# Kernel optimization log

Hardware: AMD Instinct MI355X
Metric: run time of the kernel (lower is better)

## Reference

```python
import jax, jax.numpy as jnp
import numpy as np

NUM_GROUPS = 8
NUM_HEADS = 4
EPS = 1e-5


def group_norm(x, w, b):
    # x: [B, C, H, W]; normalize over (C/G, H, W) within each of G groups
    B, C, H, W = x.shape
    xg = x.reshape(B, NUM_GROUPS, C // NUM_GROUPS, H, W)
    mean = xg.mean(axis=(2, 3, 4), keepdims=True)
    var = xg.var(axis=(2, 3, 4), keepdims=True)
    xn = ((xg - mean) * jax.lax.rsqrt(var + EPS)).reshape(B, C, H, W)
    return xn * w[None, :, None, None] + b[None, :, None, None]


def setup_inputs() -> dict:
    key = jax.random.key(0)
    ks = jax.random.split(key, 7)
    B, C, H, W = 4, 256, 64, 64
    x = jax.random.normal(ks[0], (B, C, H, W), dtype=jnp.float32)
    gn_w = jax.random.normal(ks[1], (C,), dtype=jnp.float32) * 0.1 + 1.0
    gn_b = jax.random.normal(ks[2], (C,), dtype=jnp.float32) * 0.1
    qkv_w = jax.random.normal(ks[3], (3 * C, C), dtype=jnp.float32) / np.sqrt(C)
    qkv_b = jax.random.normal(ks[4], (3 * C,), dtype=jnp.float32) * 0.02
    proj_w = jax.random.normal(ks[5], (C, C), dtype=jnp.float32) / np.sqrt(C)
    proj_b = jax.random.normal(ks[6], (C,), dtype=jnp.float32) * 0.02
    return {"x": x, "gn_w": gn_w, "gn_b": gn_b, "qkv_w": qkv_w,
            "qkv_b": qkv_b, "proj_w": proj_w, "proj_b": proj_b}


def reference(x, gn_w, gn_b, qkv_w, qkv_b, proj_w, proj_b):
    B, C, H, W = x.shape
    nh = NUM_HEADS
    hd = C // nh
    scale = hd ** -0.5
    N = H * W

    h = group_norm(x, gn_w, gn_b)
    # 1x1 conv == channel matmul: [B, 3C, H, W]
    qkv = jnp.einsum('oc,bchw->bohw', qkv_w, h) + qkv_b[None, :, None, None]
    qkv = qkv.reshape(B, 3, nh, hd, N)  # matches torch .view(B,3,nh,hd,HW)
    q, k, v = qkv[:, 0], qkv[:, 1], qkv[:, 2]  # each [B, nh, hd, N]

    attn = jnp.einsum('bhdn,bhdm->bhnm', q, k) * scale  # [B, nh, N, N]
    attn = jax.nn.softmax(attn, axis=-1)
    out = jnp.einsum('bhnm,bhdm->bhdn', attn, v)  # [B, nh, hd, N]
    out = out.reshape(B, C, H, W)

    proj = jnp.einsum('oc,bchw->bohw', proj_w, out) + proj_b[None, :, None, None]
    return x + proj
```

## Files before the change

kernel.cpp:

```cpp
#include <hip/hip_runtime.h>
#include <hip/hip_bf16.h>

#define BB   4
#define CC   256
#define NN   4096
#define NH   4
#define HD   64
#define NG   8
#define GSZ  32
#define EPSV 1e-5f
#define SCALE_L2E 0.18033688f

typedef __bf16 bf16x8 __attribute__((ext_vector_type(8)));
typedef float  f32x4  __attribute__((ext_vector_type(4)));

#define MFMA16(a, b, c)  __builtin_amdgcn_mfma_f32_16x16x32_bf16((a), (b), (c), 0, 0, 0)

#if __has_builtin(__builtin_amdgcn_exp2f)
#define EXP2F __builtin_amdgcn_exp2f
#else
#define EXP2F exp2f
#endif

#define WAITV(n)  asm volatile("s_waitcnt vmcnt(" #n ")" ::: "memory")
#define WAITL0    asm volatile("s_waitcnt lgkmcnt(0)" ::: "memory")
#define SBAR      __builtin_amdgcn_s_barrier()
#define SCHED0    __builtin_amdgcn_sched_barrier(0)

__device__ inline unsigned short f2bf(float f) {
    unsigned int u = __float_as_uint(f);
    u += 0x7fffu + ((u >> 16) & 1u);
    return (unsigned short)(u >> 16);
}

__device__ __forceinline__ bf16x8 pk8(const f32x4& p0, const f32x4& p1) {
    alignas(16) unsigned int u[4];
    u[0] = __builtin_amdgcn_perm(__float_as_uint(p0[1]), __float_as_uint(p0[0]), 0x07060302u);
    u[1] = __builtin_amdgcn_perm(__float_as_uint(p0[3]), __float_as_uint(p0[2]), 0x07060302u);
    u[2] = __builtin_amdgcn_perm(__float_as_uint(p1[1]), __float_as_uint(p1[0]), 0x07060302u);
    u[3] = __builtin_amdgcn_perm(__float_as_uint(p1[3]), __float_as_uint(p1[2]), 0x07060302u);
    return *reinterpret_cast<bf16x8*>(u);
}

__device__ __forceinline__ void async_ld16(void* lds, const void* g) {
    __builtin_amdgcn_global_load_lds(
        (const __attribute__((address_space(1))) unsigned int*)g,
        (__attribute__((address_space(3))) unsigned int*)lds, 16, 0, 0);
}

__global__ void k_prep(const float* __restrict__ x, float* __restrict__ stats,
                       const float* __restrict__ wp, unsigned short* __restrict__ op) {
    int blk = blockIdx.x;
    int t = threadIdx.x;
    if (blk >= 256) {
        int i = (blk - 256) * 256 + t;
        if (i < CC * CC) op[i] = f2bf(wp[i]);
        return;
    }
    int b = blk >> 6, g = (blk >> 3) & 7, s = blk & 7;
    const float* p = x + ((size_t)(b * CC + g * GSZ)) * NN + s * 16384;
    float s0 = 0.f, s1 = 0.f;
    #pragma unroll
    for (int i = 0; i < 64; ++i) { float v = p[i * 256 + t]; s0 += v; s1 += v * v; }
    #pragma unroll
    for (int m = 1; m <= 32; m <<= 1) { s0 += __shfl_xor(s0, m); s1 += __shfl_xor(s1, m); }
    __shared__ float ls[8];
    int w = t >> 6;
    if ((t & 63) == 0) { ls[w * 2] = s0; ls[w * 2 + 1] = s1; }
    __syncthreads();
    if (t == 0) {
        float a0 = ls[0] + ls[2] + ls[4] + ls[6];
        float a1 = ls[1] + ls[3] + ls[5] + ls[7];
        stats[((b * NG + g) * 8 + s) * 2 + 0] = a0;
        stats[((b * NG + g) * 8 + s) * 2 + 1] = a1;
    }
}

__global__ void __launch_bounds__(256)
k_tab(const float* __restrict__ wq, const float* __restrict__ gw, const float* __restrict__ gb,
      const float* __restrict__ qb, const float* __restrict__ stats,
      unsigned short* __restrict__ wqp, float* __restrict__ biasq) {
    int o = blockIdx.x, b = blockIdx.y, c = threadIdx.x;
    int g = c >> 5;
    float s0 = 0.f, s1 = 0.f;
    #pragma unroll
    for (int s = 0; s < 8; ++s) {
        s0 += stats[((b * NG + g) * 8 + s) * 2 + 0];
        s1 += stats[((b * NG + g) * 8 + s) * 2 + 1];
    }
    float mean = s0 * (1.0f / 131072.0f);
    float var  = s1 * (1.0f / 131072.0f) - mean * mean;
    float inv  = rsqrtf(var + EPSV);
    float Ac = gw[c] * inv;
    float Bc = gb[c] - mean * Ac;
    float w = wq[o * CC + c];
    wqp[((size_t)b * 768 + o) * CC + c] = f2bf(w * Ac);
    float p = w * Bc;
    #pragma unroll
    for (int m = 1; m <= 32; m <<= 1) p += __shfl_xor(p, m);
    __shared__ float ls[4];
    if ((c & 63) == 0) ls[c >> 6] = p;
    __syncthreads();
    if (c == 0) biasq[b * 768 + o] = qb[o] + ls[0] + ls[1] + ls[2] + ls[3];
}

__global__ void __launch_bounds__(256)
k_qkv(const float* __restrict__ x, const unsigned short* __restrict__ wqp,
      const float* __restrict__ biasq,
      unsigned short* __restrict__ qt, unsigned short* __restrict__ kt,
      unsigned short* __restrict__ vt) {
    int bx = blockIdx.x, by = blockIdx.y;
    int t = threadIdx.x, wave = t >> 6, lane = t & 63;
    int l15 = lane & 15, quad = lane >> 4;
    int wm = wave >> 1, wn = wave & 1;

    __shared__ alignas(16) unsigned char smem[49152];

    int nn0 = bx * 128;
    int b = nn0 >> 12, nbase = nn0 & 4095;

    const char* Ag = (const char*)wqp + (size_t)b * 393216 + (size_t)by * 65536;
    int row0 = t >> 2, slot = t & 3;
    size_t a0 = (size_t)row0 * 512 + slot * 16;
    size_t a1 = a0 + 64 * 512;
    unsigned int dstA = wave * 1024;

    int colsrc = (((lane & 31) * 16) - 32 * wave) & 511;
    const char* xrow = (const char*)x +
        (((size_t)(b * CC) + (wave * 8 + (lane >> 5))) * NN + nbase) * 4 + colsrc;

    auto stage = [&](int buf, int kk) {
        async_ld16(smem + buf * 8192 + dstA,        Ag + a0 + (size_t)kk * 64);
        async_ld16(smem + buf * 8192 + 4096 + dstA, Ag + a1 + (size_t)kk * 64);
        const char* bs = xrow + (size_t)kk * 32 * NN * 4;
        unsigned char* bd = smem + 16384 + buf * 16384 + wave * 4096;
        async_ld16(bd,        bs);
        async_ld16(bd + 1024, bs + (size_t)2 * NN * 4);
        async_ld16(bd + 2048, bs + (size_t)4 * NN * 4);
        async_ld16(bd + 3072, bs + (size_t)6 * NN * 4);
    };

    int colr[4];
    #pragma unroll
    for (int f = 0; f < 4; ++f)
        colr[f] = (((wn * 64 + f * 16 + l15) * 4) + quad * 32) & 511;

    f32x4 acc[4][4];
    #pragma unroll
    for (int i = 0; i < 4; ++i)
        #pragma unroll
        for (int j = 0; j < 4; ++j) acc[i][j] = (f32x4){0.f, 0.f, 0.f, 0.f};

    stage(0, 0);
    stage(1, 1);

    for (int kk = 0; kk < 8; ++kk) {
        if (kk < 7) { WAITV(6); } else { WAITV(0); }
        SCHED0;
        SBAR;
        SCHED0;
        int cur = kk & 1;
        bf16x8 af[4], bf[4];
        #pragma unroll
        for (int f = 0; f < 4; ++f)
            af[f] = *reinterpret_cast<const bf16x8*>(smem + cur * 8192 + (wm * 64 + f * 16 + l15) * 64 + quad * 16);
        #pragma unroll
        for (int f = 0; f < 4; ++f) {
            const unsigned char* fb = smem + 16384 + cur * 16384 + quad * 4096 + colr[f];
            alignas(16) unsigned int u[4];
            #pragma unroll
            for (int jj = 0; jj < 4; ++jj) {
                float xl = *reinterpret_cast<const float*>(fb + (2 * jj) * 512);
                float xh = *reinterpret_cast<const float*>(fb + (2 * jj + 1) * 512);
                asm("v_cvt_pk_bf16_f32 %0, %1, %2" : "=v"(u[jj]) : "v"(xl), "v"(xh));
            }
            bf[f] = *reinterpret_cast<const bf16x8*>(u);
        }
        #pragma unroll
        for (int fm = 0; fm < 4; ++fm)
            #pragma unroll
            for (int fn = 0; fn < 4; ++fn)
                acc[fm][fn] = MFMA16(af[fm], bf[fn], acc[fm][fn]);
        WAITL0;
        SCHED0;
        SBAR;
        SCHED0;
        if (kk < 6) stage(cur, kk + 2);
    }

    int s = by >> 1;
    if (s < 2) {
        #pragma unroll
        for (int fm = 0; fm < 4; ++fm) {
            int o = by * 128 + wm * 64 + fm * 16 + quad * 4;
            int h = (o >> 6) & 3, d0 = o & 63;
            float bias[4];
            #pragma unroll
            for (int r = 0; r < 4; ++r) bias[r] = biasq[b * 768 + o + r];
            #pragma unroll
            for (int fn = 0; fn < 4; ++fn) {
                int n = nbase + wn * 64 + fn * 16 + l15;
                alignas(8) unsigned short o4[4];
                if (s == 0) {
                    #pragma unroll
                    for (int r = 0; r < 4; ++r) o4[r] = f2bf((acc[fm][fn][r] + bias[r]) * SCALE_L2E);
                    *reinterpret_cast<uint2*>(qt + (((size_t)(b * NH + h) * NN) + n) * HD + d0) =
                        *reinterpret_cast<const uint2*>(o4);
                } else {
                    #pragma unroll
                    for (int r = 0; r < 4; ++r) o4[r] = f2bf(acc[fm][fn][r] + bias[r]);
                    *reinterpret_cast<uint2*>(kt + (((size_t)(b * NH + h) * NN) + n) * HD + d0) =
                        *reinterpret_cast<const uint2*>(o4);
                }
            }
        }
    } else {
        unsigned short* vtile = (unsigned short*)smem;
        #pragma unroll
        for (int fm = 0; fm < 4; ++fm) {
            int o  = by * 128 + wm * 64 + fm * 16 + quad * 4;
            int ol = wm * 64 + fm * 16 + quad * 4;
            float bias[4];
            #pragma unroll
            for (int r = 0; r < 4; ++r) bias[r] = biasq[b * 768 + o + r];
            #pragma unroll
            for (int fn = 0; fn < 4; ++fn) {
                int nl = wn * 64 + fn * 16 + l15;
                #pragma unroll
                for (int r = 0; r < 4; ++r)
                    vtile[(ol + r) * 132 + nl] = f2bf(acc[fm][fn][r] + bias[r]);
            }
        }
        __syncthreads();
        int hbase = (by - 4) * 2;
        #pragma unroll
        for (int pass = 0; pass < 8; ++pass) {
            int row  = pass * 16 + (t >> 4);
            int col0 = (t & 15) * 8;
            int nb = (col0 & ~31) | ((col0 & 16) >> 1) | ((col0 & 8) >> 1);
            const unsigned short* src = vtile + row * 132 + nb;
            uint2 lo = *reinterpret_cast<const uint2*>(src);
            uint2 hi = *reinterpret_cast<const uint2*>(src + 16);
            uint4 o4 = make_uint4(lo.x, lo.y, hi.x, hi.y);
            int h = hbase + (row >> 6), d = row & 63;
            *reinterpret_cast<uint4*>(vt + ((size_t)(b * NH + h) * HD + d) * NN + nbase + col0) = o4;
        }
    }
}

__global__ void __launch_bounds__(256, 4)
k_attn(const unsigned short* __restrict__ qt, const unsigned short* __restrict__ kt,
       const unsigned short* __restrict__ vt,
       unsigned short* __restrict__ op0, unsigned short* __restrict__ op1,
       float* __restrict__ lip) {
    int bh = blockIdx.y;
    int split = blockIdx.z;
    int t = threadIdx.x, wave = t >> 6, lane = t & 63;
    int l15 = lane & 15, quad = lane >> 4;
    int qbase = blockIdx.x * 128 + wave * 32;
    int kbase = split * 2048;
    const unsigned short* qp = qt + (size_t)bh * NN * HD;
    const unsigned short* kp = kt + (size_t)bh * NN * HD;
    const unsigned short* vp = vt + (size_t)bh * HD * NN;

    __shared__ alignas(16) unsigned char kbuf[2][8192];
    __shared__ alignas(16) unsigned char vbuf[2][8192];

    int lr8 = lane >> 3, lc8 = lane & 7;
    int swz = lc8 ^ lr8;
    const char* ksrc = (const char*)kp + (size_t)(kbase + wave * 16 + lr8) * 128 + swz * 16;
    const char* vsrc = (const char*)vp + (size_t)(wave * 16 + lr8) * 8192 + (size_t)kbase * 2 + swz * 16;
    unsigned int dstw = wave * 2048;

    auto stage = [&](int buf) {
        async_ld16(kbuf[buf] + dstw,        ksrc);
        async_ld16(kbuf[buf] + dstw + 1024, ksrc + 1024);
        ksrc += 8192;
        async_ld16(vbuf[buf] + dstw,        vsrc);
        async_ld16(vbuf[buf] + dstw + 1024, vsrc + 8 * 8192);
        vsrc += 128;
    };

    bf16x8 qaA0 = *reinterpret_cast<const bf16x8*>(qp + (size_t)(qbase + l15) * HD + quad * 8);
    bf16x8 qaA1 = *reinterpret_cast<const bf16x8*>(qp + (size_t)(qbase + l15) * HD + 32 + quad * 8);
    bf16x8 qaB0 = *reinterpret_cast<const bf16x8*>(qp + (size_t)(qbase + 16 + l15) * HD + quad * 8);
    bf16x8 qaB1 = *reinterpret_cast<const bf16x8*>(qp + (size_t)(qbase + 16 + l15) * HD + 32 + quad * 8);

    const f32x4 Z4 = (f32x4){0.f, 0.f, 0.f, 0.f};
    bf16x8 vone;
    #pragma unroll
    for (int i = 0; i < 8; ++i) vone[i] = (__bf16)1.0f;

    f32x4 OA[4], OB[4];
    #pragma unroll
    for (int i = 0; i < 4; ++i) { OA[i] = Z4; OB[i] = Z4; }
    f32x4 liAA = Z4, liBB = Z4;

    int sx = l15 & 7;

    auto compute = [&](const unsigned char* kb, const unsigned char* vbb) {
        f32x4 sA0[2], sA1[2], sB0[2], sB1[2];
        __builtin_amdgcn_s_setprio(1);
        #pragma unroll
        for (int s = 0; s < 2; ++s) {
            int r0 = (s * 32 + l15) * 128;
            bf16x8 k00 = *reinterpret_cast<const bf16x8*>(kb + r0 + ((quad ^ sx) * 16));
            bf16x8 k01 = *reinterpret_cast<const bf16x8*>(kb + r0 + (((quad + 4) ^ sx) * 16));
            bf16x8 k10 = *reinterpret_cast<const bf16x8*>(kb + r0 + 2048 + ((quad ^ sx) * 16));
            bf16x8 k11 = *reinterpret_cast<const bf16x8*>(kb + r0 + 2048 + (((quad + 4) ^ sx) * 16));
            sA0[s] = MFMA16(k00, qaA0, Z4);  sA0[s] = MFMA16(k01, qaA1, sA0[s]);
            sA1[s] = MFMA16(k10, qaA0, Z4);  sA1[s] = MFMA16(k11, qaA1, sA1[s]);
            sB0[s] = MFMA16(k00, qaB0, Z4);  sB0[s] = MFMA16(k01, qaB1, sB0[s]);
            sB1[s] = MFMA16(k10, qaB0, Z4);  sB1[s] = MFMA16(k11, qaB1, sB1[s]);
        }
        __builtin_amdgcn_s_setprio(0);
        #pragma unroll
        for (int s = 0; s < 2; ++s) {
            f32x4 pA0, pA1, pB0, pB1;
            #pragma unroll
            for (int r = 0; r < 4; ++r) {
                pA0[r] = EXP2F(sA0[s][r]);  pA1[r] = EXP2F(sA1[s][r]);
                pB0[r] = EXP2F(sB0[s][r]);  pB1[r] = EXP2F(sB1[s][r]);
            }
            bf16x8 fA = pk8(pA0, pA1);
            bf16x8 fB = pk8(pB0, pB1);

            __builtin_amdgcn_s_setprio(1);
            liAA = MFMA16(fA, vone, liAA);
            liBB = MFMA16(fB, vone, liBB);

            #pragma unroll
            for (int dc = 0; dc < 4; ++dc) {
                const unsigned char* vrow = vbb + (dc * 16 + l15) * 128;
                bf16x8 vv = *reinterpret_cast<const bf16x8*>(vrow + (((s * 4 + quad) ^ sx) * 16));
                OA[dc] = MFMA16(fA, vv, OA[dc]);
                OB[dc] = MFMA16(fB, vv, OB[dc]);
            }
            __builtin_amdgcn_s_setprio(0);
        }
    };

    stage(0);
    __syncthreads();

    for (int p = 0; p < 16; ++p) {
        stage(1);
        compute(kbuf[0], vbuf[0]);
        __syncthreads();
        if (p < 15) stage(0);
        compute(kbuf[1], vbuf[1]);
        __syncthreads();
    }

    unsigned short* op = split ? op1 : op0;
    int b = bh >> 2, h = bh & 3;
    #pragma unroll
    for (int dc = 0; dc < 4; ++dc) {
        #pragma unroll
        for (int r = 0; r < 4; ++r) {
            int qA = qbase + quad * 4 + r;
            op[((size_t)(b * NN) + qA) * CC + h * HD + dc * 16 + l15]      = f2bf(OA[dc][r]);
            op[((size_t)(b * NN) + qA + 16) * CC + h * HD + dc * 16 + l15] = f2bf(OB[dc][r]);
        }
    }
    float* lp = lip + (size_t)split * (16 * NN) + (size_t)bh * NN + qbase;
    if (l15 == 0) {
        #pragma unroll
        for (int r = 0; r < 4; ++r) {
            lp[quad * 4 + r]      = liAA[r];
            lp[16 + quad * 4 + r] = liBB[r];
        }
    }
}

__global__ void __launch_bounds__(256)
k_proj(const unsigned short* __restrict__ ao, const unsigned short* __restrict__ p1,
       const float* __restrict__ lip,
       const unsigned short* __restrict__ wp, const float* __restrict__ pb,
       const float* __restrict__ x, float* __restrict__ out) {
    int bx = blockIdx.x, by = blockIdx.y;
    int t = threadIdx.x, wave = t >> 6, lane = t & 63;
    int l15 = lane & 15, quad = lane >> 4;
    int wm = wave >> 1, wn = wave & 1;

    __shared__ alignas(16) unsigned char At[2][4096];
    __shared__ alignas(16) unsigned char Bt[2][4096];

    const char* Ag = (const char*)wp + (size_t)by * 32768;
    int row0 = t >> 2, slot = t & 3;
    size_t a0 = (size_t)row0 * 512 + slot * 16;
    unsigned int dst0 = wave * 1024;

    int gtok = bx * 64 + row0;
    int b = gtok >> 12, n = gtok & 4095;
    size_t obase = ((size_t)(b * NN) + n) * CC + slot * 8;
    float inv[4];
    #pragma unroll
    for (int h = 0; h < 4; ++h) {
        size_t lb = (size_t)(b * 4 + h) * NN + n;
        inv[h] = 1.0f / (lip[lb] + lip[lb + (size_t)16 * NN]);
    }

    auto stageA = [&](int buf, int kk) {
        async_ld16(At[buf] + dst0, Ag + a0 + (size_t)kk * 64);
    };
    uint4 eu0, eu1, ou0, ou1;
    auto loadB = [&](uint4& r0, uint4& r1, int kk) {
        r0 = *reinterpret_cast<const uint4*>(ao + obase + kk * 32);
        r1 = *reinterpret_cast<const uint4*>(p1 + obase + kk * 32);
    };
    auto writeB = [&](int buf, const uint4& r0, const uint4& r1, float iv) {
        const unsigned short* q0 = reinterpret_cast<const unsigned short*>(&r0);
        const unsigned short* q1 = reinterpret_cast<const unsigned short*>(&r1);
        alignas(16) unsigned short o8[8];
        #pragma unroll
        for (int i = 0; i < 8; ++i) {
            float f0 = __uint_as_float((unsigned)q0[i] << 16);
            float f1 = __uint_as_float((unsigned)q1[i] << 16);
            o8[i] = f2bf((f0 + f1) * iv);
        }
        *reinterpret_cast<uint4*>(Bt[buf] + row0 * 64 + slot * 16) =
            *reinterpret_cast<const uint4*>(o8);
    };

    f32x4 acc[2][2];
    #pragma unroll
    for (int i = 0; i < 2; ++i)
        #pragma unroll
        for (int j = 0; j < 2; ++j) acc[i][j] = (f32x4){0.f, 0.f, 0.f, 0.f};

    loadB(eu0, eu1, 0);
    stageA(0, 0);
    loadB(ou0, ou1, 1);

    #pragma unroll
    for (int k2 = 0; k2 < 4; ++k2) {
        {
            const int kk = 2 * k2;
            WAITV(2);
            SCHED0;
            writeB(0, eu0, eu1, inv[kk >> 1]);
            WAITL0;
            SCHED0;
            SBAR;
            SCHED0;
            if (kk < 7) stageA(1, kk + 1);
            if (kk < 6) loadB(eu0, eu1, kk + 2);
            bf16x8 af[2], bf[2];
            #pragma unroll
            for (int f = 0; f < 2; ++f) {
                af[f] = *reinterpret_cast<const bf16x8*>(At[0] + (wm * 32 + f * 16 + l15) * 64 + quad * 16);
                bf[f] = *reinterpret_cast<const bf16x8*>(Bt[0] + (wn * 32 + f * 16 + l15) * 64 + quad * 16);
            }
            #pragma unroll
            for (int fm = 0; fm < 2; ++fm)
                #pragma unroll
                for (int fn = 0; fn < 2; ++fn)
                    acc[fm][fn] = MFMA16(af[fm], bf[fn], acc[fm][fn]);
        }
        {
            const int kk = 2 * k2 + 1;
            if (kk < 7) { WAITV(2); } else { WAITV(0); }
            SCHED0;
            writeB(1, ou0, ou1, inv[kk >> 1]);
            WAITL0;
            SCHED0;
            SBAR;
            SCHED0;
            if (kk < 7) stageA(0, kk + 1);
            if (kk < 6) loadB(ou0, ou1, kk + 2);
            bf16x8 af[2], bf[2];
            #pragma unroll
            for (int f = 0; f < 2; ++f) {
                af[f] = *reinterpret_cast<const bf16x8*>(At[1] + (wm * 32 + f * 16 + l15) * 64 + quad * 16);
                bf[f] = *reinterpret_cast<const bf16x8*>(Bt[1] + (wn * 32 + f * 16 + l15) * 64 + quad * 16);
            }
            #pragma unroll
            for (int fm = 0; fm < 2; ++fm)
                #pragma unroll
                for (int fn = 0; fn < 2; ++fn)
                    acc[fm][fn] = MFMA16(af[fm], bf[fn], acc[fm][fn]);
        }
    }

    int nn0 = bx * 64;
    int bb = nn0 >> 12, nbase = nn0 & 4095;
    #pragma unroll
    for (int fm = 0; fm < 2; ++fm) {
        int o = by * 64 + wm * 32 + fm * 16 + quad * 4;
        float bias[4];
        #pragma unroll
        for (int r = 0; r < 4; ++r) bias[r] = pb[o + r];
        #pragma unroll
        for (int fn = 0; fn < 2; ++fn) {
            int nc = nbase + wn * 32 + fn * 16 + l15;
            #pragma unroll
            for (int r = 0; r < 4; ++r) {
                size_t idx = ((size_t)(bb * CC + o + r)) * NN + nc;
                out[idx] = acc[fm][fn][r] + bias[r] + x[idx];
            }
        }
    }
}

extern "C" void kernel_launch(void* const* d_in, const int* in_sizes, int n_in,
                              void* d_out, int out_size, void* d_ws, size_t ws_size,
                              hipStream_t stream) {
    const float* x     = (const float*)d_in[0];
    const float* gw    = (const float*)d_in[1];
    const float* gb    = (const float*)d_in[2];
    const float* qkvw  = (const float*)d_in[3];
    const float* qkvb  = (const float*)d_in[4];
    const float* projw = (const float*)d_in[5];
    const float* projb = (const float*)d_in[6];
    float* out = (float*)d_out;

    char* w = (char*)d_ws;
    size_t off = 0;
    unsigned short* qt = (unsigned short*)(w + off); off += (size_t)BB * NH * NN * HD * 2;
    unsigned short* kt = (unsigned short*)(w + off); off += (size_t)BB * NH * NN * HD * 2;
    unsigned short* vt = (unsigned short*)(w + off); off += (size_t)BB * NH * HD * NN * 2;
    unsigned short* ao = (unsigned short*)(w + off); off += (size_t)BB * NN * CC * 2;
    unsigned short* pt1 = (unsigned short*)(w + off); off += (size_t)BB * NN * CC * 2;
    unsigned short* wqp = (unsigned short*)(w + off); off += (size_t)BB * 3 * CC * CC * 2;
    float* biasq = (float*)(w + off); off += (size_t)BB * 3 * CC * sizeof(float);
    unsigned short* wpb = (unsigned short*)(w + off); off += (size_t)CC * CC * 2;
    float* stats = (float*)(w + off); off += (size_t)BB * NG * 8 * 2 * sizeof(float);
    float* lip   = (float*)(w + off); off += (size_t)2 * 16 * NN * sizeof(float);

    k_prep<<<512, 256, 0, stream>>>(x, stats, projw, wpb);
    k_tab<<<dim3(3 * CC, BB), 256, 0, stream>>>(qkvw, gw, gb, qkvb, stats, wqp, biasq);
    k_qkv<<<dim3(BB * NN / 128, 6), 256, 0, stream>>>(x, wqp, biasq, qt, kt, vt);
    k_attn<<<dim3(NN / 128, BB * NH, 2), 256, 0, stream>>>(qt, kt, vt, ao, pt1, lip);
    k_proj<<<dim3(BB * NN / 64, CC / 64), 256, 0, stream>>>(ao, pt1, lip, wpb, projb, x, out);
}
```

Measured before the change: 180.0 us.

## Remove split-KV attention and normalize output inside attention kernel

The attention kernel now processes all keys per query block instead of splitting keys into two halves. It applies the reciprocal row sum before writing bf16 output, which removes the second partial-output buffer and the row-sum buffer. The projection GEMM becomes a simple double-buffered async load of both operands, and the weight-table kernel handles all batches per block. The trade-off is half as many attention blocks, which reduces parallelism and occupancy across the GPU.

```diff
diff --git a/kernel.cpp b/kernel.cpp
--- a/kernel.cpp
+++ b/kernel.cpp
@@ -80,28 +80,32 @@
 k_tab(const float* __restrict__ wq, const float* __restrict__ gw, const float* __restrict__ gb,
       const float* __restrict__ qb, const float* __restrict__ stats,
       unsigned short* __restrict__ wqp, float* __restrict__ biasq) {
-    int o = blockIdx.x, b = blockIdx.y, c = threadIdx.x;
+    int o = blockIdx.x, c = threadIdx.x;
     int g = c >> 5;
-    float s0 = 0.f, s1 = 0.f;
-    #pragma unroll
-    for (int s = 0; s < 8; ++s) {
-        s0 += stats[((b * NG + g) * 8 + s) * 2 + 0];
-        s1 += stats[((b * NG + g) * 8 + s) * 2 + 1];
-    }
-    float mean = s0 * (1.0f / 131072.0f);
-    float var  = s1 * (1.0f / 131072.0f) - mean * mean;
-    float inv  = rsqrtf(var + EPSV);
-    float Ac = gw[c] * inv;
-    float Bc = gb[c] - mean * Ac;
     float w = wq[o * CC + c];
-    wqp[((size_t)b * 768 + o) * CC + c] = f2bf(w * Ac);
-    float p = w * Bc;
-    #pragma unroll
-    for (int m = 1; m <= 32; m <<= 1) p += __shfl_xor(p, m);
-    __shared__ float ls[4];
-    if ((c & 63) == 0) ls[c >> 6] = p;
+    float gwc = gw[c], gbc = gb[c];
+    __shared__ float ls[4][4];
+    #pragma unroll
+    for (int b = 0; b < 4; ++b) {
+        float s0 = 0.f, s1 = 0.f;
+        #pragma unroll
+        for (int s = 0; s < 8; ++s) {
+            s0 += stats[((b * NG + g) * 8 + s) * 2 + 0];
+            s1 += stats[((b * NG + g) * 8 + s) * 2 + 1];
+        }
+        float mean = s0 * (1.0f / 131072.0f);
+        float var  = s1 * (1.0f / 131072.0f) - mean * mean;
+        float inv  = rsqrtf(var + EPSV);
+        float Ac = gwc * inv;
+        float Bc = gbc - mean * Ac;
+        wqp[((size_t)b * 768 + o) * CC + c] = f2bf(w * Ac);
+        float p = w * Bc;
+        #pragma unroll
+        for (int m = 1; m <= 32; m <<= 1) p += __shfl_xor(p, m);
+        if ((c & 63) == 0) ls[b][c >> 6] = p;
+    }
     __syncthreads();
-    if (c == 0) biasq[b * 768 + o] = qb[o] + ls[0] + ls[1] + ls[2] + ls[3];
+    if (c < 4) biasq[c * 768 + o] = qb[o] + ls[c][0] + ls[c][1] + ls[c][2] + ls[c][3];
 }
 
 __global__ void __launch_bounds__(256)
@@ -250,15 +254,11 @@
 
 __global__ void __launch_bounds__(256, 4)
 k_attn(const unsigned short* __restrict__ qt, const unsigned short* __restrict__ kt,
-       const unsigned short* __restrict__ vt,
-       unsigned short* __restrict__ op0, unsigned short* __restrict__ op1,
-       float* __restrict__ lip) {
+       const unsigned short* __restrict__ vt, unsigned short* __restrict__ ao) {
     int bh = blockIdx.y;
-    int split = blockIdx.z;
     int t = threadIdx.x, wave = t >> 6, lane = t & 63;
     int l15 = lane & 15, quad = lane >> 4;
     int qbase = blockIdx.x * 128 + wave * 32;
-    int kbase = split * 2048;
     const unsigned short* qp = qt + (size_t)bh * NN * HD;
     const unsigned short* kp = kt + (size_t)bh * NN * HD;
     const unsigned short* vp = vt + (size_t)bh * HD * NN;
@@ -268,8 +268,8 @@
 
     int lr8 = lane >> 3, lc8 = lane & 7;
     int swz = lc8 ^ lr8;
-    const char* ksrc = (const char*)kp + (size_t)(kbase + wave * 16 + lr8) * 128 + swz * 16;
-    const char* vsrc = (const char*)vp + (size_t)(wave * 16 + lr8) * 8192 + (size_t)kbase * 2 + swz * 16;
+    const char* ksrc = (const char*)kp + (size_t)(wave * 16 + lr8) * 128 + swz * 16;
+    const char* vsrc = (const char*)vp + (size_t)(wave * 16 + lr8) * 8192 + swz * 16;
     unsigned int dstw = wave * 2048;
 
     auto stage = [&](int buf) {
@@ -343,41 +343,35 @@
     stage(0);
     __syncthreads();
 
-    for (int p = 0; p < 16; ++p) {
+    for (int p = 0; p < 32; ++p) {
         stage(1);
         compute(kbuf[0], vbuf[0]);
         __syncthreads();
-        if (p < 15) stage(0);
+        if (p < 31) stage(0);
         compute(kbuf[1], vbuf[1]);
         __syncthreads();
     }
 
-    unsigned short* op = split ? op1 : op0;
+    f32x4 rA, rB;
+    #pragma unroll
+    for (int r = 0; r < 4; ++r) { rA[r] = 1.0f / liAA[r]; rB[r] = 1.0f / liBB[r]; }
+
     int b = bh >> 2, h = bh & 3;
     #pragma unroll
     for (int dc = 0; dc < 4; ++dc) {
         #pragma unroll
         for (int r = 0; r < 4; ++r) {
             int qA = qbase + quad * 4 + r;
-            op[((size_t)(b * NN) + qA) * CC + h * HD + dc * 16 + l15]      = f2bf(OA[dc][r]);
-            op[((size_t)(b * NN) + qA + 16) * CC + h * HD + dc * 16 + l15] = f2bf(OB[dc][r]);
-        }
-    }
-    float* lp = lip + (size_t)split * (16 * NN) + (size_t)bh * NN + qbase;
-    if (l15 == 0) {
-        #pragma unroll
-        for (int r = 0; r < 4; ++r) {
-            lp[quad * 4 + r]      = liAA[r];
-            lp[16 + quad * 4 + r] = liBB[r];
+            ao[((size_t)(b * NN) + qA) * CC + h * HD + dc * 16 + l15]      = f2bf(OA[dc][r] * rA[r]);
+            ao[((size_t)(b * NN) + qA + 16) * CC + h * HD + dc * 16 + l15] = f2bf(OB[dc][r] * rB[r]);
         }
     }
 }
 
 __global__ void __launch_bounds__(256)
-k_proj(const unsigned short* __restrict__ ao, const unsigned short* __restrict__ p1,
-       const float* __restrict__ lip,
-       const unsigned short* __restrict__ wp, const float* __restrict__ pb,
-       const float* __restrict__ x, float* __restrict__ out) {
+k_proj(const unsigned short* __restrict__ ao, const unsigned short* __restrict__ wp,
+       const float* __restrict__ pb, const float* __restrict__ x,
+       float* __restrict__ out) {
     int bx = blockIdx.x, by = blockIdx.y;
     int t = threadIdx.x, wave = t >> 6, lane = t & 63;
     int l15 = lane & 15, quad = lane >> 4;
@@ -387,41 +381,16 @@
     __shared__ alignas(16) unsigned char Bt[2][4096];
 
     const char* Ag = (const char*)wp + (size_t)by * 32768;
+    const char* Bg = (const char*)ao + (size_t)bx * 32768;
     int row0 = t >> 2, slot = t & 3;
     size_t a0 = (size_t)row0 * 512 + slot * 16;
     unsigned int dst0 = wave * 1024;
 
-    int gtok = bx * 64 + row0;
-    int b = gtok >> 12, n = gtok & 4095;
-    size_t obase = ((size_t)(b * NN) + n) * CC + slot * 8;
-    float inv[4];
-    #pragma unroll
-    for (int h = 0; h < 4; ++h) {
-        size_t lb = (size_t)(b * 4 + h) * NN + n;
-        inv[h] = 1.0f / (lip[lb] + lip[lb + (size_t)16 * NN]);
-    }
-
-    auto stageA = [&](int buf, int kk) {
-        async_ld16(At[buf] + dst0, Ag + a0 + (size_t)kk * 64);
+    auto stage = [&](int buf, int kk) {
+        size_t ko = (size_t)kk * 64;
+        async_ld16(At[buf] + dst0, Ag + a0 + ko);
+        async_ld16(Bt[buf] + dst0, Bg + a0 + ko);
     };
-    uint4 eu0, eu1, ou0, ou1;
-    auto loadB = [&](uint4& r0, uint4& r1, int kk) {
-        r0 = *reinterpret_cast<const uint4*>(ao + obase + kk * 32);
-        r1 = *reinterpret_cast<const uint4*>(p1 + obase + kk * 32);
-    };
-    auto writeB = [&](int buf, const uint4& r0, const uint4& r1, float iv) {
-        const unsigned short* q0 = reinterpret_cast<const unsigned short*>(&r0);
-        const unsigned short* q1 = reinterpret_cast<const unsigned short*>(&r1);
-        alignas(16) unsigned short o8[8];
-        #pragma unroll
-        for (int i = 0; i < 8; ++i) {
-            float f0 = __uint_as_float((unsigned)q0[i] << 16);
-            float f1 = __uint_as_float((unsigned)q1[i] << 16);
-            o8[i] = f2bf((f0 + f1) * iv);
-        }
-        *reinterpret_cast<uint4*>(Bt[buf] + row0 * 64 + slot * 16) =
-            *reinterpret_cast<const uint4*>(o8);
-    };
 
     f32x4 acc[2][2];
     #pragma unroll
@@ -429,62 +398,35 @@
         #pragma unroll
         for (int j = 0; j < 2; ++j) acc[i][j] = (f32x4){0.f, 0.f, 0.f, 0.f};
 
-    loadB(eu0, eu1, 0);
-    stageA(0, 0);
-    loadB(ou0, ou1, 1);
-
-    #pragma unroll
-    for (int k2 = 0; k2 < 4; ++k2) {
-        {
-            const int kk = 2 * k2;
-            WAITV(2);
-            SCHED0;
-            writeB(0, eu0, eu1, inv[kk >> 1]);
-            WAITL0;
-            SCHED0;
-            SBAR;
-            SCHED0;
-            if (kk < 7) stageA(1, kk + 1);
-            if (kk < 6) loadB(eu0, eu1, kk + 2);
-            bf16x8 af[2], bf[2];
-            #pragma unroll
-            for (int f = 0; f < 2; ++f) {
-                af[f] = *reinterpret_cast<const bf16x8*>(At[0] + (wm * 32 + f * 16 + l15) * 64 + quad * 16);
-                bf[f] = *reinterpret_cast<const bf16x8*>(Bt[0] + (wn * 32 + f * 16 + l15) * 64 + quad * 16);
-            }
-            #pragma unroll
-            for (int fm = 0; fm < 2; ++fm)
-                #pragma unroll
-                for (int fn = 0; fn < 2; ++fn)
-                    acc[fm][fn] = MFMA16(af[fm], bf[fn], acc[fm][fn]);
-        }
-        {
-            const int kk = 2 * k2 + 1;
-            if (kk < 7) { WAITV(2); } else { WAITV(0); }
-            SCHED0;
-            writeB(1, ou0, ou1, inv[kk >> 1]);
-            WAITL0;
-            SCHED0;
-            SBAR;
-            SCHED0;
-            if (kk < 7) stageA(0, kk + 1);
-            if (kk < 6) loadB(ou0, ou1, kk + 2);
-            bf16x8 af[2], bf[2];
-            #pragma unroll
-            for (int f = 0; f < 2; ++f) {
-                af[f] = *reinterpret_cast<const bf16x8*>(At[1] + (wm * 32 + f * 16 + l15) * 64 + quad * 16);
-                bf[f] = *reinterpret_cast<const bf16x8*>(Bt[1] + (wn * 32 + f * 16 + l15) * 64 + quad * 16);
-            }
-            #pragma unroll
-            for (int fm = 0; fm < 2; ++fm)
-                #pragma unroll
-                for (int fn = 0; fn < 2; ++fn)
-                    acc[fm][fn] = MFMA16(af[fm], bf[fn], acc[fm][fn]);
-        }
+    stage(0, 0);
+    stage(1, 1);
+
+    for (int kk = 0; kk < 8; ++kk) {
+        if (kk < 7) { WAITV(2); } else { WAITV(0); }
+        SCHED0;
+        SBAR;
+        SCHED0;
+        int cur = kk & 1;
+        bf16x8 af[2], bf[2];
+        #pragma unroll
+        for (int f = 0; f < 2; ++f) {
+            af[f] = *reinterpret_cast<const bf16x8*>(At[cur] + (wm * 32 + f * 16 + l15) * 64 + quad * 16);
+            bf[f] = *reinterpret_cast<const bf16x8*>(Bt[cur] + (wn * 32 + f * 16 + l15) * 64 + quad * 16);
+        }
+        #pragma unroll
+        for (int fm = 0; fm < 2; ++fm)
+            #pragma unroll
+            for (int fn = 0; fn < 2; ++fn)
+                acc[fm][fn] = MFMA16(af[fm], bf[fn], acc[fm][fn]);
+        WAITL0;
+        SCHED0;
+        SBAR;
+        SCHED0;
+        if (kk < 6) stage(cur, kk + 2);
     }
 
     int nn0 = bx * 64;
-    int bb = nn0 >> 12, nbase = nn0 & 4095;
+    int b = nn0 >> 12, nbase = nn0 & 4095;
     #pragma unroll
     for (int fm = 0; fm < 2; ++fm) {
         int o = by * 64 + wm * 32 + fm * 16 + quad * 4;
@@ -493,10 +435,10 @@
         for (int r = 0; r < 4; ++r) bias[r] = pb[o + r];
         #pragma unroll
         for (int fn = 0; fn < 2; ++fn) {
-            int nc = nbase + wn * 32 + fn * 16 + l15;
+            int n = nbase + wn * 32 + fn * 16 + l15;
             #pragma unroll
             for (int r = 0; r < 4; ++r) {
-                size_t idx = ((size_t)(bb * CC + o + r)) * NN + nc;
+                size_t idx = ((size_t)(b * CC + o + r)) * NN + n;
                 out[idx] = acc[fm][fn][r] + bias[r] + x[idx];
             }
         }
@@ -521,16 +463,14 @@
     unsigned short* kt = (unsigned short*)(w + off); off += (size_t)BB * NH * NN * HD * 2;
     unsigned short* vt = (unsigned short*)(w + off); off += (size_t)BB * NH * HD * NN * 2;
     unsigned short* ao = (unsigned short*)(w + off); off += (size_t)BB * NN * CC * 2;
-    unsigned short* pt1 = (unsigned short*)(w + off); off += (size_t)BB * NN * CC * 2;
     unsigned short* wqp = (unsigned short*)(w + off); off += (size_t)BB * 3 * CC * CC * 2;
     float* biasq = (float*)(w + off); off += (size_t)BB * 3 * CC * sizeof(float);
     unsigned short* wpb = (unsigned short*)(w + off); off += (size_t)CC * CC * 2;
     float* stats = (float*)(w + off); off += (size_t)BB * NG * 8 * 2 * sizeof(float);
-    float* lip   = (float*)(w + off); off += (size_t)2 * 16 * NN * sizeof(float);
 
     k_prep<<<512, 256, 0, stream>>>(x, stats, projw, wpb);
-    k_tab<<<dim3(3 * CC, BB), 256, 0, stream>>>(qkvw, gw, gb, qkvb, stats, wqp, biasq);
+    k_tab<<<768, 256, 0, stream>>>(qkvw, gw, gb, qkvb, stats, wqp, biasq);
     k_qkv<<<dim3(BB * NN / 128, 6), 256, 0, stream>>>(x, wqp, biasq, qt, kt, vt);
-    k_attn<<<dim3(NN / 128, BB * NH, 2), 256, 0, stream>>>(qt, kt, vt, ao, pt1, lip);
-    k_proj<<<dim3(BB * NN / 64, CC / 64), 256, 0, stream>>>(ao, pt1, lip, wpb, projb, x, out);
-}
+    k_attn<<<dim3(NN / 128, BB * NH), 256, 0, stream>>>(qt, kt, vt, ao);
+    k_proj<<<dim3(BB * NN / 64, CC / 64), 256, 0, stream>>>(ao, wpb, projb, x, out);
+}
```

Result: no change. 179.5 us (-0.3%).
